# Kernel optimization log

Hardware: AMD Instinct MI355X
Metric: run time of the kernel (lower is better)

## Reference

```python
import jax, jax.numpy as jnp
import numpy as np

UP = 2
CUTOFF = 1.0 / UP  # factor = 1


def make_recon_rect(N, cutoff):
    """Reconstruction low-pass rect for rfft2, shape [N, N//2+1]."""
    lo = int(N * cutoff // 2)
    hi = int(N - lo)
    r = np.ones(N, dtype=np.float32)
    r[lo + 1:hi] = 0.0
    if N % 4 == 0:
        r[lo] = 0.5
        r[hi] = 0.5
    rect2d = r[:, None] * r[None, :]          # [N, N]
    return jnp.asarray(rect2d[:, :N // 2 + 1])  # keep rfft half-spectrum


def setup_inputs() -> dict:
    key = jax.random.key(0)
    x = jax.random.normal(key, (16, 64, 128, 128), dtype=jnp.float32)
    return {"x": x}


def reference(x):
    B, C, H, W = x.shape
    Hu, Wu = H * UP, W * UP
    # zero-insertion upsample: sample at (i*UP, j*UP), zeros elsewhere
    z = jnp.zeros((B, C, Hu, Wu), dtype=x.dtype).at[:, :, ::UP, ::UP].set(x)
    rect = make_recon_rect(Wu, CUTOFF)         # [Wu, Wu//2+1]
    xf = jnp.fft.rfft2(z) * rect               # low-pass in frequency domain
    out = jnp.fft.irfft2(xf) * (UP ** 2)       # gain correction
    return out
```

## Files before the change

### kernel.cpp

```cpp
#include <hip/hip_runtime.h>


typedef __bf16 bf16x8 __attribute__((ext_vector_type(8)));
typedef float  f32x4  __attribute__((ext_vector_type(4)));

#define PI_F 3.14159265358979323846f

__device__ __forceinline__ unsigned short f2bf(float x) {
    unsigned int b = __float_as_uint(x);
    return (unsigned short)((b + 0x7FFFu + ((b >> 16) & 1u)) >> 16);
}

__device__ __forceinline__ float gfun(int j) {
    int d = 2 * (j & 127) + 1;
    float th = PI_F * (float)d * (1.0f / 256.0f);
    float s  = ((d & 3) == 1) ? 1.0f : -1.0f;
    return s * cosf(th) / (128.0f * sinf(th));
}

__device__ __forceinline__ int etswz(int row) {
    return (((row & 7) ^ (((row >> 3) & 3) << 1) ^ (((row >> 5) & 1) << 2)) << 4);
}

__global__ __launch_bounds__(512)
void init_ghtab(unsigned short* __restrict__ ghtab)
{
    const int t    = threadIdx.x;
    const int lane = t & 63;
    const int l15  = lane & 15;
    const int l4   = lane >> 4;
    const int dd   = t >> 6;
    const int base = l15 - 8 * l4 + 16 * dd;
    unsigned short u[8];
    #pragma unroll
    for (int e = 0; e < 8; ++e) u[e] = f2bf(gfun(base - e));
    *(ushort4*)&ghtab[t * 8]     = make_ushort4(u[0], u[1], u[2], u[3]);
    *(ushort4*)&ghtab[t * 8 + 4] = make_ushort4(u[4], u[5], u[6], u[7]);
}

__global__ __launch_bounds__(512, 4)
void upsample_fused(const float* __restrict__ xin, float* __restrict__ out,
                    const unsigned short* __restrict__ ghtab)
{
    __shared__ __align__(16) unsigned short Et[128 * 128];

    const int tid  = threadIdx.x;
    const int lane = tid & 63;
    const int w    = tid >> 6;
    const int l15  = lane & 15;
    const int l4   = lane >> 4;

    const long long img = blockIdx.x >> 1;
    const int cb        = blockIdx.x & 1;
    const float* __restrict__ xim = xin + img * (128LL * 128LL);
    float*       __restrict__ oim = out + img * (256LL * 256LL);

    const int r = 16 * w + l15;
    const float* __restrict__ xrow = xim + r * 128;

    float4 xlo[4], xhi[4];
    #pragma unroll
    for (int t = 0; t < 4; ++t) {
        xlo[t] = *(const float4*)&xrow[32 * t + 8 * l4];
        xhi[t] = *(const float4*)&xrow[32 * t + 8 * l4 + 4];
    }

    bf16x8 ghc[8];
    #pragma unroll
    for (int v = 0; v < 8; ++v) {
        const int dd = (v + 4 * cb) & 7;
        ghc[v] = *(const bf16x8*)&ghtab[(dd * 64 + lane) * 8];
    }

    bf16x8 xa[4];
    #pragma unroll
    for (int t = 0; t < 4; ++t) {
        union { bf16x8 v; unsigned short u[8]; } H;
        H.u[0] = f2bf(xlo[t].x); H.u[1] = f2bf(xlo[t].y);
        H.u[2] = f2bf(xlo[t].z); H.u[3] = f2bf(xlo[t].w);
        H.u[4] = f2bf(xhi[t].x); H.u[5] = f2bf(xhi[t].y);
        H.u[6] = f2bf(xhi[t].z); H.u[7] = f2bf(xhi[t].w);
        xa[t] = H.v;
        if ((t >> 1) == cb) {
            const int tt = t & 1;
            #pragma unroll
            for (int e = 0; e < 8; ++e) {
                const int row = 64 * tt + 16 * l4 + 2 * e;
                Et[row * 128 + (((2 * r) ^ etswz(row)) >> 1)] = H.u[e];
            }
        }
    }

    float* __restrict__ orow = oim + (2 * r) * 256 + 128 * cb;
    #pragma unroll
    for (int mt = 0; mt < 4; ++mt) {
        f32x4 acc = {0.f, 0.f, 0.f, 0.f};
        #pragma unroll
        for (int t = 0; t < 4; ++t)
            acc = __builtin_amdgcn_mfma_f32_16x16x32_bf16(ghc[(mt - 2 * t) & 7],
                                                          xa[t], acc, 0, 0, 0);
        const int i0l = 16 * mt + 4 * l4;
        float4 xc = *(const float4*)&xrow[64 * cb + i0l];
        float4 o0 = make_float4(xc.x, acc[0], xc.y, acc[1]);
        float4 o1 = make_float4(xc.z, acc[2], xc.w, acc[3]);
        *(float4*)&orow[2 * i0l]     = o0;
        *(float4*)&orow[2 * i0l + 4] = o1;
        #pragma unroll
        for (int q = 0; q < 4; ++q) {
            const int row = 2 * (i0l + q) + 1;
            Et[row * 128 + (((2 * r) ^ etswz(row)) >> 1)] = f2bf(acc[q]);
        }
    }
    __syncthreads();

    {
        const int pa = w & 3;
        const int mh = w >> 2;
        bf16x8 gbd[4];
        #pragma unroll
        for (int d = 0; d < 4; ++d) {
            const int dd = (pa + 2 * d) & 7;
            gbd[d] = *(const bf16x8*)&ghtab[(dd * 64 + lane) * 8];
        }
        float* __restrict__ prowA = oim + (2 * (16 * pa + l15) + 1) * 256 + 128 * cb;
        float* __restrict__ prowB = oim + (2 * (16 * (pa + 4) + l15) + 1) * 256 + 128 * cb;
        #pragma unroll
        for (int mci = 0; mci < 4; ++mci) {
            const int mc = 4 * mh + mci;
            const int row = 16 * mc + l15;
            const char* erow = (const char*)Et + row * 256;
            const int sw = etswz(row);
            f32x4 aA = {0.f, 0.f, 0.f, 0.f};
            f32x4 aB = {0.f, 0.f, 0.f, 0.f};
            #pragma unroll
            for (int t = 0; t < 4; ++t) {
                bf16x8 ef = *(const bf16x8*)(erow + (((64 * t + 16 * l4)) ^ sw));
                aA = __builtin_amdgcn_mfma_f32_16x16x32_bf16(ef, gbd[(-t) & 3], aA, 0, 0, 0);
                aB = __builtin_amdgcn_mfma_f32_16x16x32_bf16(ef, gbd[(2 - t) & 3], aB, 0, 0, 0);
            }
            float4 oA = make_float4(aA[0], aA[1], aA[2], aA[3]);
            float4 oB = make_float4(aB[0], aB[1], aB[2], aB[3]);
            *(float4*)&prowA[16 * mc + 4 * l4] = oA;
            *(float4*)&prowB[16 * mc + 4 * l4] = oB;
        }
    }
}

extern "C" void kernel_launch(void* const* d_in, const int* in_sizes, int n_in,
                              void* d_out, int out_size, void* d_ws, size_t ws_size,
                              hipStream_t stream)
{
    (void)n_in; (void)out_size; (void)ws_size;
    const float* x = (const float*)d_in[0];
    float* out = (float*)d_out;
    int nimg = in_sizes[0] / (128 * 128);

    unsigned short* ghtab = (unsigned short*)d_ws;
    hipLaunchKernelGGL(init_ghtab, dim3(1), dim3(512), 0, stream, ghtab);
    hipLaunchKernelGGL(upsample_fused, dim3(nimg * 2), dim3(512), 0, stream, x, out, ghtab);
}
```

Before: 95.36 us.

## Split fused upsample into even-row kernel and odd-row kernel via global output

Splits the single fused kernel into two launches. The first computes the even output rows, horizontal interpolation only, and writes them to global memory. The second reads those even rows back from the output buffer, stages them in shared memory as bf16, and computes the odd rows. This removes the duplicated per-column-half horizontal work and the shared staging from the first pass, which may ease register and LDS pressure. In exchange it adds an extra global read of half the output and another kernel launch.

```diff
diff --git a/kernel.cpp b/kernel.cpp
--- a/kernel.cpp
+++ b/kernel.cpp
@@ -38,9 +38,66 @@
     *(ushort4*)&ghtab[t * 8 + 4] = make_ushort4(u[4], u[5], u[6], u[7]);
 }
 
-__global__ __launch_bounds__(512, 4)
-void upsample_fused(const float* __restrict__ xin, float* __restrict__ out,
-                    const unsigned short* __restrict__ ghtab)
+__global__ __launch_bounds__(256)
+void k1_even(const float* __restrict__ xin, float* __restrict__ out,
+             const unsigned short* __restrict__ ghtab)
+{
+    const int tid  = threadIdx.x;
+    const int lane = tid & 63;
+    const int w    = tid >> 6;
+    const int l15  = lane & 15;
+    const int l4   = lane >> 4;
+
+    const long long img = blockIdx.x >> 1;
+    const int rh        = blockIdx.x & 1;
+    const float* __restrict__ xim = xin + img * (128LL * 128LL);
+    float*       __restrict__ oim = out + img * (256LL * 256LL);
+
+    const int r = 64 * rh + 16 * w + l15;
+    const float* __restrict__ xrow = xim + r * 128;
+
+    float4 xlo[4], xhi[4];
+    #pragma unroll
+    for (int t = 0; t < 4; ++t) {
+        xlo[t] = *(const float4*)&xrow[32 * t + 8 * l4];
+        xhi[t] = *(const float4*)&xrow[32 * t + 8 * l4 + 4];
+    }
+
+    bf16x8 ghc[8];
+    #pragma unroll
+    for (int v = 0; v < 8; ++v)
+        ghc[v] = *(const bf16x8*)&ghtab[(v * 64 + lane) * 8];
+
+    bf16x8 xa[4];
+    #pragma unroll
+    for (int t = 0; t < 4; ++t) {
+        union { bf16x8 v; unsigned short u[8]; } H;
+        H.u[0] = f2bf(xlo[t].x); H.u[1] = f2bf(xlo[t].y);
+        H.u[2] = f2bf(xlo[t].z); H.u[3] = f2bf(xlo[t].w);
+        H.u[4] = f2bf(xhi[t].x); H.u[5] = f2bf(xhi[t].y);
+        H.u[6] = f2bf(xhi[t].z); H.u[7] = f2bf(xhi[t].w);
+        xa[t] = H.v;
+    }
+
+    float* __restrict__ orow = oim + (2 * r) * 256;
+    #pragma unroll
+    for (int mt = 0; mt < 8; ++mt) {
+        f32x4 acc = {0.f, 0.f, 0.f, 0.f};
+        #pragma unroll
+        for (int t = 0; t < 4; ++t)
+            acc = __builtin_amdgcn_mfma_f32_16x16x32_bf16(ghc[(mt - 2 * t) & 7],
+                                                          xa[t], acc, 0, 0, 0);
+        const int i0 = 16 * mt + 4 * l4;
+        float4 xc = *(const float4*)&xrow[i0];
+        float4 o0 = make_float4(xc.x, acc[0], xc.y, acc[1]);
+        float4 o1 = make_float4(xc.z, acc[2], xc.w, acc[3]);
+        *(float4*)&orow[2 * i0]     = o0;
+        *(float4*)&orow[2 * i0 + 4] = o1;
+    }
+}
+
+__global__ __launch_bounds__(512)
+void k2_odd(float* __restrict__ out, const unsigned short* __restrict__ ghtab)
 {
     __shared__ __align__(16) unsigned short Et[128 * 128];
 
@@ -52,63 +109,19 @@
 
     const long long img = blockIdx.x >> 1;
     const int cb        = blockIdx.x & 1;
-    const float* __restrict__ xim = xin + img * (128LL * 128LL);
-    float*       __restrict__ oim = out + img * (256LL * 256LL);
+    float* __restrict__ oim = out + img * (256LL * 256LL);
 
-    const int r = 16 * w + l15;
-    const float* __restrict__ xrow = xim + r * 128;
-
-    float4 xlo[4], xhi[4];
     #pragma unroll
-    for (int t = 0; t < 4; ++t) {
-        xlo[t] = *(const float4*)&xrow[32 * t + 8 * l4];
-        xhi[t] = *(const float4*)&xrow[32 * t + 8 * l4 + 4];
-    }
-
-    bf16x8 ghc[8];
-    #pragma unroll
-    for (int v = 0; v < 8; ++v) {
-        const int dd = (v + 4 * cb) & 7;
-        ghc[v] = *(const bf16x8*)&ghtab[(dd * 64 + lane) * 8];
-    }
-
-    bf16x8 xa[4];
-    #pragma unroll
-    for (int t = 0; t < 4; ++t) {
-        union { bf16x8 v; unsigned short u[8]; } H;
-        H.u[0] = f2bf(xlo[t].x); H.u[1] = f2bf(xlo[t].y);
-        H.u[2] = f2bf(xlo[t].z); H.u[3] = f2bf(xlo[t].w);
-        H.u[4] = f2bf(xhi[t].x); H.u[5] = f2bf(xhi[t].y);
-        H.u[6] = f2bf(xhi[t].z); H.u[7] = f2bf(xhi[t].w);
-        xa[t] = H.v;
-        if ((t >> 1) == cb) {
-            const int tt = t & 1;
-            #pragma unroll
-            for (int e = 0; e < 8; ++e) {
-                const int row = 64 * tt + 16 * l4 + 2 * e;
-                Et[row * 128 + (((2 * r) ^ etswz(row)) >> 1)] = H.u[e];
-            }
-        }
-    }
-
-    float* __restrict__ orow = oim + (2 * r) * 256 + 128 * cb;
-    #pragma unroll
-    for (int mt = 0; mt < 4; ++mt) {
-        f32x4 acc = {0.f, 0.f, 0.f, 0.f};
+    for (int k = 0; k < 8; ++k) {
+        const int fidx = k * 512 + tid;
+        const int m    = fidx >> 5;
+        const int c4   = fidx & 31;
+        float4 v = *(const float4*)&oim[(2 * m) * 256 + 128 * cb + 4 * c4];
+        float vv[4] = {v.x, v.y, v.z, v.w};
         #pragma unroll
-        for (int t = 0; t < 4; ++t)
-            acc = __builtin_amdgcn_mfma_f32_16x16x32_bf16(ghc[(mt - 2 * t) & 7],
-                                                          xa[t], acc, 0, 0, 0);
-        const int i0l = 16 * mt + 4 * l4;
-        float4 xc = *(const float4*)&xrow[64 * cb + i0l];
-        float4 o0 = make_float4(xc.x, acc[0], xc.y, acc[1]);
-        float4 o1 = make_float4(xc.z, acc[2], xc.w, acc[3]);
-        *(float4*)&orow[2 * i0l]     = o0;
-        *(float4*)&orow[2 * i0l + 4] = o1;
-        #pragma unroll
-        for (int q = 0; q < 4; ++q) {
-            const int row = 2 * (i0l + q) + 1;
-            Et[row * 128 + (((2 * r) ^ etswz(row)) >> 1)] = f2bf(acc[q]);
+        for (int e = 0; e < 4; ++e) {
+            const int row = 4 * c4 + e;
+            Et[row * 128 + (((2 * m) ^ etswz(row)) >> 1)] = f2bf(vv[e]);
         }
     }
     __syncthreads();
@@ -134,7 +147,7 @@
             f32x4 aB = {0.f, 0.f, 0.f, 0.f};
             #pragma unroll
             for (int t = 0; t < 4; ++t) {
-                bf16x8 ef = *(const bf16x8*)(erow + (((64 * t + 16 * l4)) ^ sw));
+                bf16x8 ef = *(const bf16x8*)(erow + ((64 * t + 16 * l4) ^ sw));
                 aA = __builtin_amdgcn_mfma_f32_16x16x32_bf16(ef, gbd[(-t) & 3], aA, 0, 0, 0);
                 aB = __builtin_amdgcn_mfma_f32_16x16x32_bf16(ef, gbd[(2 - t) & 3], aB, 0, 0, 0);
             }
@@ -157,5 +170,6 @@
 
     unsigned short* ghtab = (unsigned short*)d_ws;
     hipLaunchKernelGGL(init_ghtab, dim3(1), dim3(512), 0, stream, ghtab);
-    hipLaunchKernelGGL(upsample_fused, dim3(nimg * 2), dim3(512), 0, stream, x, out, ghtab);
+    hipLaunchKernelGGL(k1_even, dim3(nimg * 2), dim3(256), 0, stream, x, out, ghtab);
+    hipLaunchKernelGGL(k2_odd,  dim3(nimg * 2), dim3(512), 0, stream, out, ghtab);
 }
```

Measured after the change: 105.1 us. 10.2% more time.
